# Performance work log

Measured on AMD Instinct MI355X. Metric: run time of the kernel, lower is better.

## Reference

```python
import jax, jax.numpy as jnp
import numpy as np

# J6 incidence matrix for Plucker coordinates (constant buffer in the torch module)
_J6 = jnp.array([[0, 0, 0, 0, 0, 1],
                 [0, 0, 0, 0, -1, 0],
                 [0, 0, 0, 1, 0, 0],
                 [0, 0, 1, 0, 0, 0],
                 [0, -1, 0, 0, 0, 0],
                 [1, 0, 0, 0, 0, 0]], dtype=jnp.float32)

# combinations(range(4), 2) index pairs for the exterior product
_PI = np.array([0, 0, 0, 1, 1, 2])
_PJ = np.array([1, 2, 3, 2, 3, 3])


def plucker_lines(p1, p2):
    # p1, p2: (..., 4) -> normalized Plucker 6-vectors (..., 6)
    lines = p1[..., _PI] * p2[..., _PJ] - p1[..., _PJ] * p2[..., _PI]
    n = jnp.linalg.norm(lines, axis=-1, keepdims=True)
    return lines / jnp.maximum(n, 1e-12)


def setup_inputs() -> dict:
    key = jax.random.key(0)
    ks = jax.random.split(key, 6)
    B, T, D, H = 1, 2048, 1024, 16
    s = D ** -0.5
    x = jax.random.normal(ks[0], (B, T, D), jnp.float32)
    Wqkv = jax.random.normal(ks[1], (D, 3 * D), jnp.float32) * s
    bqkv = jnp.zeros((3 * D,), jnp.float32)
    W1p = jax.random.normal(ks[2], (D, 4 * H), jnp.float32) * s
    W2p = jax.random.normal(ks[3], (D, 4 * H), jnp.float32) * s
    plucker_scale = jnp.full((H,), 0.1, jnp.float32)
    Wout = jax.random.normal(ks[4], (D, D), jnp.float32) * s
    bout = jnp.zeros((D,), jnp.float32)
    return {"x": x, "Wqkv": Wqkv, "bqkv": bqkv, "W1p": W1p, "W2p": W2p,
            "plucker_scale": plucker_scale, "Wout": Wout, "bout": bout}


def reference(x, Wqkv, bqkv, W1p, W2p, plucker_scale, Wout, bout):
    B, T, D = x.shape
    H = plucker_scale.shape[0]
    dh = D // H

    qkv = (x @ Wqkv + bqkv).reshape(B, T, 3, H, dh)
    q = jnp.transpose(qkv[:, :, 0], (0, 2, 1, 3))  # [B,H,T,dh]
    k = jnp.transpose(qkv[:, :, 1], (0, 2, 1, 3))
    v = jnp.transpose(qkv[:, :, 2], (0, 2, 1, 3))

    std_logits = jnp.einsum('bhid,bhjd->bhij', q, k) * (dh ** -0.5)

    p1 = (x @ W1p).reshape(B, T, H, 4)
    p2 = (x @ W2p).reshape(B, T, H, 4)
    lines_h = jnp.transpose(plucker_lines(p1, p2), (0, 2, 1, 3))  # [B,H,T,6]
    Jlines = lines_h @ _J6.T                                       # [B,H,T,6]
    plucker_bias = jnp.einsum('bhic,bhjc->bhij', lines_h, Jlines)  # [B,H,T,T]

    logits = std_logits + plucker_bias * plucker_scale[None, :, None, None]
    causal = jnp.triu(jnp.ones((T, T), bool), 1)
    logits = jnp.where(causal[None, None], -jnp.inf, logits)
    attn = jax.nn.softmax(logits, axis=-1)

    out = jnp.einsum('bhij,bhjd->bhid', attn, v)
    out = jnp.transpose(out, (0, 2, 1, 3)).reshape(B, T, D)
    return out @ Wout + bout
```

## Files before the change

### kernel.cpp

```cpp
#include <hip/hip_runtime.h>

typedef unsigned short u16;
typedef unsigned int u32;
typedef __attribute__((ext_vector_type(8))) __bf16 bf16x8;
typedef __attribute__((ext_vector_type(4))) float f32x4;
typedef __attribute__((ext_vector_type(4))) u16 u16x4;

#define MFMA16(a, b, c) __builtin_amdgcn_mfma_f32_16x16x32_bf16((a), (b), (c), 0, 0, 0)

static __device__ __forceinline__ u16 f2b(float f) {
  union { float f; u32 u; } v; v.f = f;
  u32 u = v.u;
  return (u16)((u + 0x7FFFu + ((u >> 16) & 1u)) >> 16);
}

static __device__ __forceinline__ u32 pack2(float a, float b) {
  u32 r;
  asm("v_cvt_pk_bf16_f32 %0, %1, %2" : "=v"(r) : "v"(a), "v"(b));
  return r;
}

static __device__ __forceinline__ float exp2fast(float x) {
#if defined(__has_builtin) && __has_builtin(__builtin_amdgcn_exp2f)
  return __builtin_amdgcn_exp2f(x);
#else
  return __expf(x * 0.6931471805599453f);
#endif
}

static __device__ __forceinline__ void gload16(const u16* gp, u16* lp) {
  __builtin_amdgcn_global_load_lds((__attribute__((address_space(1))) void*)(u16*)gp,
                                   (__attribute__((address_space(3))) void*)lp, 16, 0, 0);
}

__global__ __launch_bounds__(256) void k_prep(const float* __restrict__ Wqkv, const float* __restrict__ Wout,
                                              const float* __restrict__ W1p, const float* __restrict__ W2p,
                                              const float* __restrict__ x,
                                              u16* __restrict__ WB, u16* __restrict__ WoT,
                                              u16* __restrict__ xb) {
  const int b = blockIdx.x;
  const int t = threadIdx.x;
  if (b < 1024) {
    __shared__ float tile[64][65];
    const float* src; u16* dst; int N, n0, k0;
    if (b < 768) { src = Wqkv; dst = WB;  N = 3072; n0 = (b % 48) * 64; k0 = (b / 48) * 64; }
    else { const int bb = b - 768; src = Wout; dst = WoT; N = 1024; n0 = (bb & 15) * 64; k0 = (bb >> 4) * 64; }
    const int rr = t >> 4, cc = (t & 15) << 2;
#pragma unroll
    for (int i = 0; i < 4; ++i) {
      const float4 v = *(const float4*)(src + (size_t)(k0 + rr + i * 16) * N + n0 + cc);
      tile[rr + i * 16][cc + 0] = v.x; tile[rr + i * 16][cc + 1] = v.y;
      tile[rr + i * 16][cc + 2] = v.z; tile[rr + i * 16][cc + 3] = v.w;
    }
    __syncthreads();
    const int nr = t >> 3, kc = (t & 7) << 3;
#pragma unroll
    for (int i = 0; i < 2; ++i) {
      u16 o[8];
#pragma unroll
      for (int j = 0; j < 8; ++j) o[j] = f2b(tile[kc + j][nr + i * 32]);
      *(uint4*)(dst + (size_t)(n0 + nr + i * 32) * 1024 + k0 + kc) = *(const uint4*)o;
    }
  } else if (b < 1536) {
    const int idx = (b - 1024) * 256 + t;
    const int j = idx >> 10, k = idx & 1023;
    const float v = (j < 64) ? W1p[(size_t)k * 64 + j] : W2p[(size_t)k * 64 + (j - 64)];
    WB[(size_t)3072 * 1024 + idx] = f2b(v);
  } else {
    const size_t idx = ((size_t)(b - 1536) * 256 + t) << 2;
    const float4 v = *(const float4*)(x + idx);
    u16x4 o; o.x = f2b(v.x); o.y = f2b(v.y); o.z = f2b(v.z); o.w = f2b(v.w);
    *(u16x4*)(xb + idx) = o;
  }
}

static __device__ __forceinline__ void gemm_core_128x64(const u16* __restrict__ A, const u16* __restrict__ B,
                                                        int brow, int bcol, int K,
                                                        u16* ldsA, u16* ldsB, f32x4 acc[4][2]) {
  const int tid = threadIdx.x;
  const int wave = tid >> 6, lane = tid & 63;
  const int wr = wave >> 1, wc = wave & 1;
  const int g = lane >> 4, l15 = lane & 15;

  for (int k0 = 0; k0 < K; k0 += 64) {
#pragma unroll
    for (int li = 0; li < 4; ++li) {
      const int f = li * 256 + wave * 64 + lane;
      const int row = f >> 3;
      const int slot = f & 7;
      const int gcol = ((slot ^ (row & 7)) << 3);
      gload16(A + (size_t)(brow + row) * K + k0 + gcol, ldsA + (size_t)(li * 256 + wave * 64) * 8);
    }
#pragma unroll
    for (int li = 0; li < 2; ++li) {
      const int f = li * 256 + wave * 64 + lane;
      const int row = f >> 3;
      const int slot = f & 7;
      const int gcol = ((slot ^ (row & 7)) << 3);
      gload16(B + (size_t)(bcol + row) * K + k0 + gcol, ldsB + (size_t)(li * 256 + wave * 64) * 8);
    }
    __syncthreads();
    bf16x8 af[4][2], bfr[2][2];
#pragma unroll
    for (int kk = 0; kk < 2; ++kk) {
#pragma unroll
      for (int m = 0; m < 4; ++m) {
        const int rowA = wr * 64 + m * 16 + l15;
        const int chA = (kk * 4 + g) ^ (rowA & 7);
        af[m][kk] = *(const bf16x8*)(ldsA + (size_t)rowA * 64 + chA * 8);
      }
#pragma unroll
      for (int n = 0; n < 2; ++n) {
        const int rowB = wc * 32 + n * 16 + l15;
        const int chB = (kk * 4 + g) ^ (rowB & 7);
        bfr[n][kk] = *(const bf16x8*)(ldsB + (size_t)rowB * 64 + chB * 8);
      }
    }
#pragma unroll
    for (int m = 0; m < 4; ++m)
#pragma unroll
      for (int n = 0; n < 2; ++n)
#pragma unroll
        for (int kk = 0; kk < 2; ++kk)
          acc[m][n] = MFMA16(af[m][kk], bfr[n][kk], acc[m][n]);
    __syncthreads();
  }
}

__global__ __launch_bounds__(256) void k_gemm_qkvp(const u16* __restrict__ xb, const u16* __restrict__ WB,
                                                   const float* __restrict__ bqkv,
                                                   u16* __restrict__ Qext, u16* __restrict__ Kext,
                                                   u16* __restrict__ Vt, float* __restrict__ P12) {
  __shared__ __align__(16) u16 ldsA[128 * 64];
  __shared__ __align__(16) u16 ldsB[64 * 64];
  const int bid = blockIdx.x;
  const int bn = bid % 50, bm = bid / 50;
  f32x4 acc[4][2];
#pragma unroll
  for (int m = 0; m < 4; ++m)
#pragma unroll
    for (int n = 0; n < 2; ++n) acc[m][n] = (f32x4){0.f, 0.f, 0.f, 0.f};
  gemm_core_128x64(xb, WB, bm * 128, bn * 64, 1024, ldsA, ldsB, acc);

  const int tid = threadIdx.x;
  const int wave = tid >> 6, lane = tid & 63;
  const int wr = wave >> 1, wc = wave & 1;
  const int g = lane >> 4, l15 = lane & 15;
  const int tbase = bm * 128 + wr * 64 + g * 4;
  const int cbase = bn * 64 + wc * 32 + l15;
#pragma unroll
  for (int m = 0; m < 4; ++m) {
#pragma unroll
    for (int n = 0; n < 2; ++n) {
      const int c = cbase + n * 16;
#pragma unroll
      for (int r = 0; r < 4; ++r) {
        const int t = tbase + m * 16 + r;
        float v = acc[m][n][r];
        if (c < 3072) {
          v += bqkv[c];
          const int sub = c >> 10;
          const int rem = c & 1023;
          const int hh = rem >> 6, d = rem & 63;
          if (sub == 0)      Qext[((size_t)hh * 2048 + t) * 96 + d] = f2b(v * 0.18033688f);
          else if (sub == 1) Kext[((size_t)hh * 2048 + t) * 96 + d] = f2b(v);
          else               Vt[(size_t)hh * 131072 + (size_t)(t >> 5) * 2048 + d * 32 + (t & 31)] = f2b(v);
        } else {
          P12[(size_t)t * 128 + (c - 3072)] = v;
        }
      }
    }
  }
}

__global__ __launch_bounds__(256) void k_lines(const float* __restrict__ P12, const float* __restrict__ pscale,
                                               u16* __restrict__ Qext, u16* __restrict__ Kext) {
  const int idx = blockIdx.x * 256 + threadIdx.x;
  const int t = idx >> 4, h = idx & 15;
  const float* p = P12 + (size_t)t * 128;
  const float a0 = p[h * 4 + 0], a1 = p[h * 4 + 1], a2 = p[h * 4 + 2], a3 = p[h * 4 + 3];
  const float b0 = p[64 + h * 4 + 0], b1 = p[64 + h * 4 + 1], b2 = p[64 + h * 4 + 2], b3 = p[64 + h * 4 + 3];
  float L0 = a0 * b1 - a1 * b0;
  float L1 = a0 * b2 - a2 * b0;
  float L2 = a0 * b3 - a3 * b0;
  float L3 = a1 * b2 - a2 * b1;
  float L4 = a1 * b3 - a3 * b1;
  float L5 = a2 * b3 - a3 * b2;
  const float nrm = sqrtf(L0 * L0 + L1 * L1 + L2 * L2 + L3 * L3 + L4 * L4 + L5 * L5);
  const float inv = 1.0f / fmaxf(nrm, 1e-12f);
  L0 *= inv; L1 *= inv; L2 *= inv; L3 *= inv; L4 *= inv; L5 *= inv;
  const float s = pscale[h] * 1.44269504f;
  u16* q = Qext + ((size_t)h * 2048 + t) * 96 + 64;
  u16* k = Kext + ((size_t)h * 2048 + t) * 96 + 64;
  q[0] = f2b(L0 * s); q[1] = f2b(L1 * s); q[2] = f2b(L2 * s);
  q[3] = f2b(L3 * s); q[4] = f2b(L4 * s); q[5] = f2b(L5 * s);
  k[0] = f2b(L5); k[1] = f2b(-L4); k[2] = f2b(L3);
  k[3] = f2b(L2); k[4] = f2b(-L1); k[5] = f2b(L0);
#pragma unroll
  for (int c = 6; c < 32; ++c) { q[c] = 0; k[c] = 0; }
}

__global__ __launch_bounds__(64) void k_attn(const u16* __restrict__ Qext, const u16* __restrict__ Kext,
                                             const u16* __restrict__ Vt, u16* __restrict__ AO) {
  const int bid = blockIdx.x;
  const int h = bid & 15;
  const int p = bid >> 4;
  const int lane = threadIdx.x;
  const int g = lane >> 4, l15 = lane & 15;
  const int q0A = p << 4;
  const int q0B = (127 - p) << 4;
  const int qgA = q0A + l15;
  const int qgB = q0B + l15;
  const int sA = (p >> 1) + 1;
  const int sB = ((127 - p) >> 1) + 1;
  const u16* Qh = Qext + (size_t)h * 2048 * 96;
  const u16* Kh = Kext + (size_t)h * 2048 * 96;
  const u16* Vh = Vt + (size_t)h * 131072;

  bf16x8 aqA[3], aqB[3];
#pragma unroll
  for (int ks = 0; ks < 3; ++ks) {
    aqA[ks] = *(const bf16x8*)(Qh + (size_t)qgA * 96 + ks * 32 + g * 8);
    aqB[ks] = *(const bf16x8*)(Qh + (size_t)qgB * 96 + ks * 32 + g * 8);
  }

  f32x4 accA[4], accB[4];
#pragma unroll
  for (int n = 0; n < 4; ++n) {
    accA[n] = (f32x4){0.f, 0.f, 0.f, 0.f};
    accB[n] = (f32x4){0.f, 0.f, 0.f, 0.f};
  }
  float lA = 0.f, lB = 0.f;

  const u16* Kbase = Kh + (size_t)l15 * 96 + g * 8;
  const u16* Vlane = Vh + (size_t)l15 * 32 + g * 8;

  bf16x8 kX0[3], kX1[3], kY0[3], kY1[3];
  bf16x8 avX[4], avY[4];
  f32x4 SA0c, SA1c, SB0c, SB1c, SA0n, SA1n, SB0n, SB1n;

  {
#pragma unroll
    for (int ks = 0; ks < 3; ++ks) {
      kX0[ks] = *(const bf16x8*)(Kbase + ks * 32);
      kX1[ks] = *(const bf16x8*)(Kbase + 16 * 96 + ks * 32);
    }
    SB0c = (f32x4){0.f, 0.f, 0.f, 0.f}; SB1c = SB0c; SA0c = SB0c; SA1c = SB0c;
#pragma unroll
    for (int ks = 0; ks < 3; ++ks) {
      SB0c = MFMA16(kX0[ks], aqB[ks], SB0c);
      SB1c = MFMA16(kX1[ks], aqB[ks], SB1c);
      SA0c = MFMA16(kX0[ks], aqA[ks], SA0c);
      SA1c = MFMA16(kX1[ks], aqA[ks], SA1c);
    }
    const u16* kp = Kbase + (size_t)((1 < sB) ? 1 : 0) * 32 * 96;
#pragma unroll
    for (int ks = 0; ks < 3; ++ks) {
      kY0[ks] = *(const bf16x8*)(kp + ks * 32);
      kY1[ks] = *(const bf16x8*)(kp + 16 * 96 + ks * 32);
    }
#pragma unroll
    for (int n = 0; n < 4; ++n) avX[n] = *(const bf16x8*)(Vlane + n * 512);
  }

#define GLUE(S0, S1, Q0S, QGS, LS, PBS)                                           \
  {                                                                               \
    if (jb + 31 > Q0S) {                                                          \
      _Pragma("unroll")                                                           \
      for (int r = 0; r < 4; ++r) {                                               \
        if (jb + g * 4 + r > QGS) S0[r] = -1e30f;                                 \
        if (jb + 16 + g * 4 + r > QGS) S1[r] = -1e30f;                            \
      }                                                                           \
    }                                                                             \
    _Pragma("unroll")                                                             \
    for (int r = 0; r < 4; ++r) {                                                 \
      S0[r] = exp2fast(S0[r]);                                                    \
      S1[r] = exp2fast(S1[r]);                                                    \
    }                                                                             \
    LS += ((S0[0] + S0[1]) + (S0[2] + S0[3])) + ((S1[0] + S1[1]) + (S1[2] + S1[3])); \
    u32 a0 = pack2(S0[0], S0[1]);                                                 \
    u32 a1 = pack2(S0[2], S0[3]);                                                 \
    u32 b0 = pack2(S1[0], S1[1]);                                                 \
    u32 b1 = pack2(S1[2], S1[3]);                                                 \
    asm("v_permlane32_swap_b32 %0, %1" : "+v"(a0), "+v"(b0));                     \
    asm("v_permlane16_swap_b32 %0, %1" : "+v"(a0), "+v"(b0));                     \
    asm("v_permlane32_swap_b32 %0, %1" : "+v"(a1), "+v"(b1));                     \
    asm("v_permlane16_swap_b32 %0, %1" : "+v"(a1), "+v"(b1));                     \
    PBS.u[0] = a0;                                                                \
    PBS.u[1] = a1;                                                                \
    PBS.u[2] = b0;                                                                \
    PBS.u[3] = b1;                                                                \
  }

#define ATTN_STEP(SA0C, SA1C, SB0C, SB1C, SA0N, SA1N, SB0N, SB1N, KN0, KN1, KL0, KL1, AVC, AVN) \
  {                                                                               \
    const int jb = jt * 32;                                                       \
    const int jn1 = (jt + 1 < sB) ? jt + 1 : jt;                                  \
    const int jn2 = (jt + 2 < sB) ? jt + 2 : jt;                                  \
                                     \
    SB0N = (f32x4){0.f, 0.f, 0.f, 0.f}; SB1N = SB0N;                              \
    __builtin_amdgcn_s_setprio(1);                                                \
    _Pragma("unroll")                                                             \
    for (int ks = 0; ks < 3; ++ks) {                                              \
      SB0N = MFMA16(KN0[ks], aqB[ks], SB0N);                                      \
      SB1N = MFMA16(KN1[ks], aqB[ks], SB1N);                                      \
    }                                                                             \
    if (jt + 1 < sA) {                                                            \
      SA0N = (f32x4){0.f, 0.f, 0.f, 0.f}; SA1N = SA0N;                            \
      _Pragma("unroll")                                                           \
      for (int ks = 0; ks < 3; ++ks) {                                            \
        SA0N = MFMA16(KN0[ks], aqA[ks], SA0N);                                    \
        SA1N = MFMA16(KN1[ks], aqA[ks], SA1N);                                    \
      }                                                                           \
    }                                                                             \
    __builtin_amdgcn_s_setprio(0);                                                \
                                                         \
    const u16* kp = Kbase + (size_t)jn2 * 32 * 96;                                \
    _Pragma("unroll")                                                             \
    for (int ks = 0; ks < 3; ++ks) {                                              \
      KL0[ks] = *(const bf16x8*)(kp + ks * 32);                                   \
      KL1[ks] = *(const bf16x8*)(kp + 16 * 96 + ks * 32);                         \
    }                                                                             \
                                                         \
    _Pragma("unroll")                                                             \
    for (int n = 0; n < 4; ++n)                                                   \
      AVN[n] = *(const bf16x8*)(Vlane + (size_t)jn1 * 2048 + n * 512);            \
                                                      \
    union { u32 u[4]; bf16x8 bv; } pbB, pbA;                                      \
    GLUE(SB0C, SB1C, q0B, qgB, lB, pbB);                                          \
    const bool actA = (jt < sA);                                                  \
    if (actA) GLUE(SA0C, SA1C, q0A, qgA, lA, pbA);                                \
                                                 \
    __builtin_amdgcn_s_setprio(1);                                                \
    _Pragma("unroll")                                                             \
    for (int n = 0; n < 4; ++n) accB[n] = MFMA16(AVC[n], pbB.bv, accB[n]);        \
    if (actA) {                                                                   \
      _Pragma("unroll")                                                           \
      for (int n = 0; n < 4; ++n) accA[n] = MFMA16(AVC[n], pbA.bv, accA[n]);      \
    }                                                                             \
    __builtin_amdgcn_s_setprio(0);                                                \
  }

  int jt = 0;
  for (;;) {
    ATTN_STEP(SA0c, SA1c, SB0c, SB1c, SA0n, SA1n, SB0n, SB1n, kY0, kY1, kX0, kX1, avX, avY);
    if (++jt >= sB) break;
    ATTN_STEP(SA0n, SA1n, SB0n, SB1n, SA0c, SA1c, SB0c, SB1c, kX0, kX1, kY0, kY1, avY, avX);
    if (++jt >= sB) break;
  }
#undef ATTN_STEP
#undef GLUE

  lA += __shfl_xor(lA, 16);
  lA += __shfl_xor(lA, 32);
  lB += __shfl_xor(lB, 16);
  lB += __shfl_xor(lB, 32);
  const float invA = 1.0f / lA;
  const float invB = 1.0f / lB;
  u32* dstA = (u32*)(AO + (size_t)qgA * 1024 + h * 64 + g * 4);
  u32* dstB = (u32*)(AO + (size_t)qgB * 1024 + h * 64 + g * 4);
#pragma unroll
  for (int n = 0; n < 4; ++n) {
    dstA[n * 8 + 0] = pack2(accA[n][0] * invA, accA[n][1] * invA);
    dstA[n * 8 + 1] = pack2(accA[n][2] * invA, accA[n][3] * invA);
    dstB[n * 8 + 0] = pack2(accB[n][0] * invB, accB[n][1] * invB);
    dstB[n * 8 + 1] = pack2(accB[n][2] * invB, accB[n][3] * invB);
  }
}

__global__ __launch_bounds__(256) void k_gemm_out(const u16* __restrict__ AO, const u16* __restrict__ WoT,
                                                  const float* __restrict__ bout, float* __restrict__ out) {
  __shared__ __align__(16) u16 ldsA[128 * 64];
  __shared__ __align__(16) u16 ldsB[32 * 64];
  const int bid = blockIdx.x;
  const int bn = bid & 31, bm = bid >> 5;
  const int tid = threadIdx.x;
  const int wave = tid >> 6, lane = tid & 63;
  const int wr = wave >> 1, wc = wave & 1;
  const int g = lane >> 4, l15 = lane & 15;

  f32x4 acc[4];
#pragma unroll
  for (int m = 0; m < 4; ++m) acc[m] = (f32x4){0.f, 0.f, 0.f, 0.f};

  for (int k0 = 0; k0 < 1024; k0 += 64) {
#pragma unroll
    for (int li = 0; li < 4; ++li) {
      const int f = li * 256 + wave * 64 + lane;
      const int row = f >> 3;
      const int slot = f & 7;
      const int gcol = ((slot ^ (row & 7)) << 3);
      gload16(AO + (size_t)(bm * 128 + row) * 1024 + k0 + gcol, ldsA + (size_t)(li * 256 + wave * 64) * 8);
    }
    {
      const int f = wave * 64 + lane;
      const int row = f >> 3;
      const int slot = f & 7;
      const int gcol = ((slot ^ (row & 7)) << 3);
      gload16(WoT + (size_t)(bn * 32 + row) * 1024 + k0 + gcol, ldsB + (size_t)(wave * 64) * 8);
    }
    __syncthreads();
    bf16x8 af[4][2], bfr[2];
#pragma unroll
    for (int kk = 0; kk < 2; ++kk) {
#pragma unroll
      for (int m = 0; m < 4; ++m) {
        const int rowA = wr * 64 + m * 16 + l15;
        const int chA = (kk * 4 + g) ^ (rowA & 7);
        af[m][kk] = *(const bf16x8*)(ldsA + (size_t)rowA * 64 + chA * 8);
      }
      const int rowB = wc * 16 + l15;
      const int chB = (kk * 4 + g) ^ (rowB & 7);
      bfr[kk] = *(const bf16x8*)(ldsB + (size_t)rowB * 64 + chB * 8);
    }
#pragma unroll
    for (int m = 0; m < 4; ++m)
#pragma unroll
      for (int kk = 0; kk < 2; ++kk)
        acc[m] = MFMA16(af[m][kk], bfr[kk], acc[m]);
    __syncthreads();
  }

  const int tbase = bm * 128 + wr * 64 + g * 4;
  const int c = bn * 32 + wc * 16 + l15;
  const float bb = bout[c];
#pragma unroll
  for (int m = 0; m < 4; ++m)
#pragma unroll
    for (int r = 0; r < 4; ++r) {
      const int t = tbase + m * 16 + r;
      out[(size_t)t * 1024 + c] = acc[m][r] + bb;
    }
}

extern "C" void kernel_launch(void* const* d_in, const int* in_sizes, int n_in,
                              void* d_out, int out_size, void* d_ws, size_t ws_size,
                              hipStream_t stream) {
  const float* x      = (const float*)d_in[0];
  const float* Wqkv   = (const float*)d_in[1];
  const float* bqkv   = (const float*)d_in[2];
  const float* W1p    = (const float*)d_in[3];
  const float* W2p    = (const float*)d_in[4];
  const float* pscale = (const float*)d_in[5];
  const float* Wout   = (const float*)d_in[6];
  const float* bout   = (const float*)d_in[7];
  float* out = (float*)d_out;

  char* ws = (char*)d_ws;
  u16*   WB    = (u16*)(ws + 0);
  u16*   WoT   = (u16*)(ws + 6553600);
  u16*   xb    = (u16*)(ws + 8650752);
  u16*   Qext  = (u16*)(ws + 12845056);
  u16*   Kext  = (u16*)(ws + 19136512);
  u16*   Vt    = (u16*)(ws + 25427968);
  float* P12   = (float*)(ws + 29622272);
  u16*   AO    = (u16*)(ws + 30670848);

  k_prep<<<3584, 256, 0, stream>>>(Wqkv, Wout, W1p, W2p, x, WB, WoT, xb);
  k_gemm_qkvp<<<800, 256, 0, stream>>>(xb, WB, bqkv, Qext, Kext, Vt, P12);
  k_lines<<<128, 256, 0, stream>>>(P12, pscale, Qext, Kext);
  k_attn<<<1024, 64, 0, stream>>>(Qext, Kext, Vt, AO);
  k_gemm_out<<<512, 256, 0, stream>>>(AO, WoT, bout, out);
}
```

Baseline: 97.08 us.

## Split K across two wave groups in QKV projection GEMM with LDS reduction

The QKV+Plucker projection GEMM now launches 512 threads per block. Two groups of four waves each compute half of the K dimension into separate LDS tiles, then reduce their partial accumulators through LDS before the epilogue. The goal is more latency hiding and wave parallelism per 128x64 tile without changing the grid size. The cost is double the LDS footprint, an extra reduction and barrier, and half the threads sitting idle during the epilogue. The loop body is inlined, so it is no longer shared with gemm_core.

New measurement: 103.8 us. 1.07x slower.

```diff
diff --git a/kernel.cpp b/kernel.cpp
--- a/kernel.cpp
+++ b/kernel.cpp
@@ -127,25 +127,91 @@
   }
 }
 
-__global__ __launch_bounds__(256) void k_gemm_qkvp(const u16* __restrict__ xb, const u16* __restrict__ WB,
+__global__ __launch_bounds__(512) void k_gemm_qkvp(const u16* __restrict__ xb, const u16* __restrict__ WB,
                                                    const float* __restrict__ bqkv,
                                                    u16* __restrict__ Qext, u16* __restrict__ Kext,
                                                    u16* __restrict__ Vt, float* __restrict__ P12) {
-  __shared__ __align__(16) u16 ldsA[128 * 64];
-  __shared__ __align__(16) u16 ldsB[64 * 64];
+  __shared__ __align__(16) u16 lds[24576];
   const int bid = blockIdx.x;
   const int bn = bid % 50, bm = bid / 50;
-  f32x4 acc[4][2];
-#pragma unroll
-  for (int m = 0; m < 4; ++m)
-#pragma unroll
-    for (int n = 0; n < 2; ++n) acc[m][n] = (f32x4){0.f, 0.f, 0.f, 0.f};
-  gemm_core_128x64(xb, WB, bm * 128, bn * 64, 1024, ldsA, ldsB, acc);
-
   const int tid = threadIdx.x;
   const int wave = tid >> 6, lane = tid & 63;
-  const int wr = wave >> 1, wc = wave & 1;
+  const int grp = wave >> 2, wl = wave & 3;
+  const int wr = wl >> 1, wc = wl & 1;
   const int g = lane >> 4, l15 = lane & 15;
+  u16* ldsA = lds + grp * 12288;
+  u16* ldsB = lds + grp * 12288 + 8192;
+
+  f32x4 acc[4][2];
+#pragma unroll
+  for (int m = 0; m < 4; ++m)
+#pragma unroll
+    for (int n = 0; n < 2; ++n) acc[m][n] = (f32x4){0.f, 0.f, 0.f, 0.f};
+
+  const int kbase = grp * 512;
+  for (int k0 = kbase; k0 < kbase + 512; k0 += 64) {
+#pragma unroll
+    for (int li = 0; li < 4; ++li) {
+      const int f = li * 256 + wl * 64 + lane;
+      const int row = f >> 3;
+      const int slot = f & 7;
+      const int gcol = ((slot ^ (row & 7)) << 3);
+      gload16(xb + (size_t)(bm * 128 + row) * 1024 + k0 + gcol, ldsA + (size_t)(li * 256 + wl * 64) * 8);
+    }
+#pragma unroll
+    for (int li = 0; li < 2; ++li) {
+      const int f = li * 256 + wl * 64 + lane;
+      const int row = f >> 3;
+      const int slot = f & 7;
+      const int gcol = ((slot ^ (row & 7)) << 3);
+      gload16(WB + (size_t)(bn * 64 + row) * 1024 + k0 + gcol, ldsB + (size_t)(li * 256 + wl * 64) * 8);
+    }
+    __syncthreads();
+    bf16x8 af[4][2], bfr[2][2];
+#pragma unroll
+    for (int kk = 0; kk < 2; ++kk) {
+#pragma unroll
+      for (int m = 0; m < 4; ++m) {
+        const int rowA = wr * 64 + m * 16 + l15;
+        const int chA = (kk * 4 + g) ^ (rowA & 7);
+        af[m][kk] = *(const bf16x8*)(ldsA + (size_t)rowA * 64 + chA * 8);
+      }
+#pragma unroll
+      for (int n = 0; n < 2; ++n) {
+        const int rowB = wc * 32 + n * 16 + l15;
+        const int chB = (kk * 4 + g) ^ (rowB & 7);
+        bfr[n][kk] = *(const bf16x8*)(ldsB + (size_t)rowB * 64 + chB * 8);
+      }
+    }
+#pragma unroll
+    for (int m = 0; m < 4; ++m)
+#pragma unroll
+      for (int n = 0; n < 2; ++n)
+#pragma unroll
+        for (int kk = 0; kk < 2; ++kk)
+          acc[m][n] = MFMA16(af[m][kk], bfr[n][kk], acc[m][n]);
+    __syncthreads();
+  }
+
+  float* red = (float*)lds;
+  const int t255 = tid & 255;
+  if (grp == 1) {
+#pragma unroll
+    for (int m = 0; m < 4; ++m)
+#pragma unroll
+      for (int n = 0; n < 2; ++n)
+        *(f32x4*)(red + (size_t)((m * 2 + n) * 256 + t255) * 4) = acc[m][n];
+  }
+  __syncthreads();
+  if (grp == 1) return;
+#pragma unroll
+  for (int m = 0; m < 4; ++m)
+#pragma unroll
+    for (int n = 0; n < 2; ++n) {
+      const f32x4 o = *(const f32x4*)(red + (size_t)((m * 2 + n) * 256 + t255) * 4);
+      acc[m][n] += o;
+    }
+
   const int tbase = bm * 128 + wr * 64 + g * 4;
   const int cbase = bn * 64 + wc * 32 + l15;
 #pragma unroll
@@ -457,7 +523,7 @@
   u16*   AO    = (u16*)(ws + 30670848);
 
   k_prep<<<3584, 256, 0, stream>>>(Wqkv, Wout, W1p, W2p, x, WB, WoT, xb);
-  k_gemm_qkvp<<<800, 256, 0, stream>>>(xb, WB, bqkv, Qext, Kext, Vt, P12);
+  k_gemm_qkvp<<<800, 512, 0, stream>>>(xb, WB, bqkv, Qext, Kext, Vt, P12);
   k_lines<<<128, 256, 0, stream>>>(P12, pscale, Qext, Kext);
   k_attn<<<1024, 64, 0, stream>>>(Qext, Kext, Vt, AO);
   k_gemm_out<<<512, 256, 0, stream>>>(AO, WoT, bout, out);
```
